# Performance work log

Measured on AMD Instinct MI355X. Metric: run time of the kernel, lower is better.

## Reference

```python
import jax, jax.numpy as jnp
import numpy as np

NUM_EXPERTS = 8
TOP_K = 2
DIM = 1024
HIDDEN = 4096
B, S = 4, 2048


def setup_inputs() -> dict:
    key = jax.random.key(0)
    ks = jax.random.split(key, 6)
    scale = 0.02
    x = jax.random.normal(ks[0], (B, S, DIM), dtype=jnp.float32)
    wg = jax.random.normal(ks[1], (NUM_EXPERTS, DIM), dtype=jnp.float32) * scale
    bg = jnp.zeros((NUM_EXPERTS,), dtype=jnp.float32)
    Wgate = jax.random.normal(ks[2], (NUM_EXPERTS, HIDDEN, DIM), dtype=jnp.float32) * scale
    Wup = jax.random.normal(ks[3], (NUM_EXPERTS, HIDDEN, DIM), dtype=jnp.float32) * scale
    Wdown = jax.random.normal(ks[4], (NUM_EXPERTS, DIM, HIDDEN), dtype=jnp.float32) * scale
    return {"x": x, "wg": wg, "bg": bg, "Wgate": Wgate, "Wup": Wup, "Wdown": Wdown}


def reference(x, wg, bg, Wgate, Wup, Wdown):
    b, s, d = x.shape
    xf = x.reshape(-1, d)  # [T, D]
    T = xf.shape[0]
    # --- gating: top-k over router logits, softmax over masked logits ---
    logits = xf @ wg.T + bg  # [T, E]
    vals, idx = jax.lax.top_k(logits, TOP_K)  # [T, K]
    masked = jnp.full_like(logits, -jnp.inf)
    rows = jnp.arange(T)[:, None]
    masked = masked.at[rows, idx].set(vals)
    weights = jax.nn.softmax(masked, axis=-1)  # zeros outside top-k
    # --- experts: weighted SwiGLU sum (weight is 0 for non-routed tokens,
    # so this matches the gather/scatter loop exactly) ---
    out = jnp.zeros_like(xf)
    for e in range(NUM_EXPERTS):
        g = xf @ Wgate[e].T            # [T, H]
        u = xf @ Wup[e].T              # [T, H]
        h = (g * jax.nn.sigmoid(g)) * u
        out = out + (h @ Wdown[e].T) * weights[:, e:e + 1]
    return out.reshape(b, s, d)
```

## Files before the change

kernel.cpp:

```cpp
#include <hip/hip_runtime.h>
#include <cstdint>
#include <cstddef>

typedef unsigned short ushort_t;
typedef __attribute__((ext_vector_type(8))) __bf16 bf16x8;
typedef __attribute__((ext_vector_type(8))) short  s16x8;
typedef __attribute__((ext_vector_type(4))) float  f32x4;

#define NE 8
#define DIM 1024
#define HIDDEN 4096
#define NTOK 8192
#define CAP NTOK
#define NROWS (NTOK * 2)

#define BM 128
#define BN 64
#define BK 32
#define LDP 40

static constexpr size_t WS_COUNTS  = 0;
static constexpr size_t WS_OFFSETS = 256;
static constexpr size_t WS_TOKENS  = 512;
static constexpr size_t WS_WEIGHTS = WS_TOKENS + (size_t)NE * CAP * 4;
static constexpr size_t WS_H       = ((WS_WEIGHTS + (size_t)NE * CAP * 4 + 1023) / 1024) * 1024;
static constexpr size_t H_BYTES    = (size_t)NROWS * HIDDEN * 2;
static constexpr size_t WS_XB      = WS_H + H_BYTES;
static constexpr size_t XB_BYTES   = (size_t)NTOK * DIM * 2;
static constexpr size_t W_BYTES    = (size_t)NE * HIDDEN * DIM * 2;
static constexpr size_t WS_WGB     = WS_XB + XB_BYTES;
static constexpr size_t WS_WUB     = WS_WGB + W_BYTES;
static constexpr size_t WS_WDB     = WS_WUB + W_BYTES;
static constexpr size_t WS_T1_END  = WS_WDB;
static constexpr size_t WS_T2_END  = WS_WDB + W_BYTES;

__device__ __forceinline__ ushort_t cvt_bf16(float f) {
  unsigned u = __float_as_uint(f);
  return (ushort_t)((u + 0x7FFFu + ((u >> 16) & 1u)) >> 16);
}

__device__ __forceinline__ void st8(ushort_t* dst, float4 a, float4 b) {
  s16x8 v;
  v[0] = (short)cvt_bf16(a.x); v[1] = (short)cvt_bf16(a.y);
  v[2] = (short)cvt_bf16(a.z); v[3] = (short)cvt_bf16(a.w);
  v[4] = (short)cvt_bf16(b.x); v[5] = (short)cvt_bf16(b.y);
  v[6] = (short)cvt_bf16(b.z); v[7] = (short)cvt_bf16(b.w);
  *reinterpret_cast<s16x8*>(dst) = v;
}

__device__ __forceinline__ bf16x8 ldb(const ushort_t* p) {
  union { s16x8 s; bf16x8 b; } u;
  u.s = *reinterpret_cast<const s16x8*>(p);
  return u.b;
}

__device__ __forceinline__ bf16x8 ldt(const ushort_t* base, int row, int s) {
  return ldb(base + (size_t)((row << 2) + (s ^ ((row >> 1) & 3))) * 8);
}

__device__ __forceinline__ f32x4 mfma16(bf16x8 a, bf16x8 b, f32x4 c) {
  return __builtin_amdgcn_mfma_f32_16x16x32_bf16(a, b, c, 0, 0, 0);
}

#define GLDS16(g, l)                                                     \
  __builtin_amdgcn_global_load_lds(                                      \
      (const __attribute__((address_space(1))) unsigned int*)(g),        \
      (__attribute__((address_space(3))) unsigned int*)(l), 16, 0, 0)

__global__ __launch_bounds__(256) void cvt_kernel(const float* __restrict__ s,
                                                  ushort_t* __restrict__ d, long n8) {
  long i = (long)blockIdx.x * 256 + threadIdx.x;
  long stride = (long)gridDim.x * 256;
  for (long p = i; p < n8; p += stride) {
    const float4* sp = reinterpret_cast<const float4*>(s) + 2 * p;
    float4 a = sp[0];
    float4 b = sp[1];
    st8(d + p * 8, a, b);
  }
}

__global__ __launch_bounds__(256) void gating_kernel(
    const float* __restrict__ x, const float* __restrict__ wg,
    const float* __restrict__ bg, int* __restrict__ counts,
    int* __restrict__ token_list, float* __restrict__ weight_list) {
  int gid  = blockIdx.x * blockDim.x + threadIdx.x;
  int tok  = gid >> 6;
  int lane = threadIdx.x & 63;
  if (tok >= NTOK) return;
  const float* xr = x + (size_t)tok * DIM;

  float part[NE];
#pragma unroll
  for (int e = 0; e < NE; ++e) part[e] = 0.f;
  for (int i = lane; i < DIM; i += 64) {
    float xv = xr[i];
#pragma unroll
    for (int e = 0; e < NE; ++e) part[e] = fmaf(xv, wg[e * DIM + i], part[e]);
  }
#pragma unroll
  for (int e = 0; e < NE; ++e) {
    float v = part[e];
#pragma unroll
    for (int o = 32; o > 0; o >>= 1) v += __shfl_xor(v, o, 64);
    part[e] = v + bg[e];
  }
  if (lane == 0) {
    int i0 = 0; float v0 = part[0];
#pragma unroll
    for (int e = 1; e < NE; ++e) if (part[e] > v0) { v0 = part[e]; i0 = e; }
    int i1 = -1; float v1 = -INFINITY;
#pragma unroll
    for (int e = 0; e < NE; ++e) if (e != i0 && part[e] > v1) { v1 = part[e]; i1 = e; }
    float e1 = expf(v1 - v0);
    float s  = 1.f + e1;
    float w0 = 1.f / s;
    float w1 = e1 / s;
    int s0 = atomicAdd(&counts[i0], 1);
    token_list[i0 * CAP + s0]  = tok;
    weight_list[i0 * CAP + s0] = w0;
    int s1 = atomicAdd(&counts[i1], 1);
    token_list[i1 * CAP + s1]  = tok;
    weight_list[i1 * CAP + s1] = w1;
  }
}

__global__ void prefix_kernel(const int* __restrict__ counts, int* __restrict__ offsets) {
  if (threadIdx.x == 0) {
    int acc = 0;
    for (int e = 0; e < NE; ++e) { offsets[e] = acc; acc += counts[e]; }
  }
}

__global__ __launch_bounds__(256) void stage1_kernel(
    const ushort_t* __restrict__ xb, const ushort_t* __restrict__ wgb,
    const ushort_t* __restrict__ wub, const int* __restrict__ counts,
    const int* __restrict__ offsets, const int* __restrict__ token_list,
    ushort_t* __restrict__ h) {
  const int e  = blockIdx.z;
  const int mt = blockIdx.y;
  const int nt = blockIdx.x;
  const int count = counts[e];
  if (mt * BM >= count) return;

  __shared__ __align__(16) ushort_t XsL[BM * 32];
  __shared__ __align__(16) ushort_t GsL[BN * 32];
  __shared__ __align__(16) ushort_t UsL[BN * 32];
  __shared__ int toks[BM];

  const int t = threadIdx.x;
  if (t < BM) {
    int m = mt * BM + t;
    toks[t] = token_list[e * CAP + (m < count ? m : count - 1)];
  }
  __syncthreads();

  const int wid  = t >> 6;
  const int lane = t & 63;
  const int wm   = wid & 1;
  const int wn   = wid >> 1;
  const int fr   = lane & 15;
  const int kg   = lane >> 4;

  const int uA = wid * 128 + lane;
  const int uB = uA + 64;
  const int rA = uA >> 2, sA = (uA & 3) ^ ((rA >> 1) & 3);
  const int rB = uB >> 2, sB = (uB & 3) ^ ((rB >> 1) & 3);
  const ushort_t* gxA = xb + (size_t)toks[rA] * DIM + sA * 8;
  const ushort_t* gxB = xb + (size_t)toks[rB] * DIM + sB * 8;

  const int uG = wid * 64 + lane;
  const int rG = uG >> 2, sG = (uG & 3) ^ ((rG >> 1) & 3);
  const size_t wrow = (size_t)e * HIDDEN + (size_t)nt * BN + rG;
  const ushort_t* ggp = wgb + wrow * DIM + sG * 8;
  const ushort_t* gup = wub + wrow * DIM + sG * 8;

  ushort_t* ldsXA = XsL + (size_t)(wid * 128) * 8;
  ushort_t* ldsXB = XsL + (size_t)(wid * 128 + 64) * 8;
  ushort_t* ldsG  = GsL + (size_t)(wid * 64) * 8;
  ushort_t* ldsU  = UsL + (size_t)(wid * 64) * 8;

  f32x4 accg[4][2], accu[4][2];
#pragma unroll
  for (int i = 0; i < 4; ++i)
#pragma unroll
    for (int j = 0; j < 2; ++j) { accg[i][j] = (f32x4)0.f; accu[i][j] = (f32x4)0.f; }

  for (int k0 = 0; k0 < DIM; k0 += BK) {
    GLDS16(gxA + k0, ldsXA);
    GLDS16(gxB + k0, ldsXB);
    GLDS16(ggp + k0, ldsG);
    GLDS16(gup + k0, ldsU);
    __syncthreads();

    bf16x8 bg0 = ldt(GsL, wn * 32 + fr, kg);
    bf16x8 bg1 = ldt(GsL, wn * 32 + 16 + fr, kg);
    bf16x8 bu0 = ldt(UsL, wn * 32 + fr, kg);
    bf16x8 bu1 = ldt(UsL, wn * 32 + 16 + fr, kg);
#pragma unroll
    for (int mf = 0; mf < 4; ++mf) {
      bf16x8 a = ldt(XsL, wm * 64 + mf * 16 + fr, kg);
      accg[mf][0] = mfma16(a, bg0, accg[mf][0]);
      accg[mf][1] = mfma16(a, bg1, accg[mf][1]);
      accu[mf][0] = mfma16(a, bu0, accu[mf][0]);
      accu[mf][1] = mfma16(a, bu1, accu[mf][1]);
    }
    __syncthreads();
  }

  const size_t slot0 = (size_t)offsets[e];
  const int nbase = nt * BN + wn * 32;
#pragma unroll
  for (int mf = 0; mf < 4; ++mf) {
#pragma unroll
    for (int r = 0; r < 4; ++r) {
      int ml = wm * 64 + mf * 16 + kg * 4 + r;
      int m  = mt * BM + ml;
      if (m < count) {
        size_t rowoff = (slot0 + m) * (size_t)HIDDEN + nbase;
#pragma unroll
        for (int nf = 0; nf < 2; ++nf) {
          float g  = accg[mf][nf][r];
          float uu = accu[mf][nf][r];
          float hv = g / (1.f + __expf(-g)) * uu;
          h[rowoff + nf * 16 + fr] = cvt_bf16(hv);
        }
      }
    }
  }
}

__global__ __launch_bounds__(256) void stage2_kernel(
    const ushort_t* __restrict__ h, const ushort_t* __restrict__ wdb,
    const int* __restrict__ counts, const int* __restrict__ offsets,
    const int* __restrict__ token_list, const float* __restrict__ weight_list,
    float* __restrict__ out) {
  const int e  = blockIdx.z;
  const int mt = blockIdx.y;
  const int nt = blockIdx.x;
  const int count = counts[e];
  if (mt * BM >= count) return;

  __shared__ __align__(16) ushort_t AsL[BM * 32];
  __shared__ __align__(16) ushort_t DsL[BN * 32];
  __shared__ int   toks[BM];
  __shared__ float wts[BM];

  const int t = threadIdx.x;
  if (t < BM) {
    int m  = mt * BM + t;
    int mc = m < count ? m : count - 1;
    toks[t] = token_list[e * CAP + mc];
    wts[t]  = weight_list[e * CAP + mc];
  }
  __syncthreads();

  const int wid  = t >> 6;
  const int lane = t & 63;
  const int wm   = wid & 1;
  const int wn   = wid >> 1;
  const int fr   = lane & 15;
  const int kg   = lane >> 4;

  const int slot0b = offsets[e] + mt * BM;

  const int uA = wid * 128 + lane;
  const int uB = uA + 64;
  const int rA = uA >> 2, sA = (uA & 3) ^ ((rA >> 1) & 3);
  const int rB = uB >> 2, sB = (uB & 3) ^ ((rB >> 1) & 3);
  int hrA = slot0b + rA; hrA = hrA < NROWS ? hrA : NROWS - 1;
  int hrB = slot0b + rB; hrB = hrB < NROWS ? hrB : NROWS - 1;
  const ushort_t* ghA = h + (size_t)hrA * HIDDEN + sA * 8;
  const ushort_t* ghB = h + (size_t)hrB * HIDDEN + sB * 8;

  const int uD = wid * 64 + lane;
  const int rD = uD >> 2, sD = (uD & 3) ^ ((rD >> 1) & 3);
  const ushort_t* gdp = wdb + ((size_t)e * DIM + (size_t)nt * BN + rD) * HIDDEN + sD * 8;

  ushort_t* ldsAA = AsL + (size_t)(wid * 128) * 8;
  ushort_t* ldsAB = AsL + (size_t)(wid * 128 + 64) * 8;
  ushort_t* ldsD  = DsL + (size_t)(wid * 64) * 8;

  f32x4 acc[4][2];
#pragma unroll
  for (int i = 0; i < 4; ++i)
#pragma unroll
    for (int j = 0; j < 2; ++j) acc[i][j] = (f32x4)0.f;

  for (int k0 = 0; k0 < HIDDEN; k0 += BK) {
    GLDS16(ghA + k0, ldsAA);
    GLDS16(ghB + k0, ldsAB);
    GLDS16(gdp + k0, ldsD);
    __syncthreads();

    bf16x8 b0 = ldt(DsL, wn * 32 + fr, kg);
    bf16x8 b1 = ldt(DsL, wn * 32 + 16 + fr, kg);
#pragma unroll
    for (int mf = 0; mf < 4; ++mf) {
      bf16x8 a = ldt(AsL, wm * 64 + mf * 16 + fr, kg);
      acc[mf][0] = mfma16(a, b0, acc[mf][0]);
      acc[mf][1] = mfma16(a, b1, acc[mf][1]);
    }
    __syncthreads();
  }

  const int nbase = nt * BN + wn * 32;
#pragma unroll
  for (int mf = 0; mf < 4; ++mf) {
#pragma unroll
    for (int r = 0; r < 4; ++r) {
      int ml = wm * 64 + mf * 16 + kg * 4 + r;
      int m  = mt * BM + ml;
      if (m < count) {
        int   tok = toks[ml];
        float w   = wts[ml];
        size_t o  = (size_t)tok * DIM + nbase;
#pragma unroll
        for (int nf = 0; nf < 2; ++nf) {
          atomicAdd(&out[o + nf * 16 + fr], acc[mf][nf][r] * w);
        }
      }
    }
  }
}

__global__ __launch_bounds__(256) void stage1_f32w(
    const float* __restrict__ x, const float* __restrict__ Wgate,
    const float* __restrict__ Wup, const int* __restrict__ counts,
    const int* __restrict__ offsets, const int* __restrict__ token_list,
    ushort_t* __restrict__ h) {
  const int e  = blockIdx.z;
  const int mt = blockIdx.y;
  const int nt = blockIdx.x;
  const int count = counts[e];
  if (mt * BM >= count) return;

  __shared__ __align__(16) ushort_t Xs[BM][LDP];
  __shared__ __align__(16) ushort_t Gs[BN][LDP];
  __shared__ __align__(16) ushort_t Us[BN][LDP];
  __shared__ int toks[BM];

  const int t = threadIdx.x;
  if (t < BM) {
    int m = mt * BM + t;
    toks[t] = token_list[e * CAP + (m < count ? m : count - 1)];
  }
  __syncthreads();

  const float* Wg = Wgate + (size_t)e * HIDDEN * DIM + (size_t)(nt * BN) * DIM;
  const float* Wu = Wup   + (size_t)e * HIDDEN * DIM + (size_t)(nt * BN) * DIM;

  const int wid  = t >> 6;
  const int lane = t & 63;
  const int wm   = wid & 1;
  const int wn   = wid >> 1;
  const int fr   = lane & 15;
  const int kg   = lane >> 4;

  f32x4 accg[4][2], accu[4][2];
#pragma unroll
  for (int i = 0; i < 4; ++i)
#pragma unroll
    for (int j = 0; j < 2; ++j) { accg[i][j] = (f32x4)0.f; accu[i][j] = (f32x4)0.f; }

  const int sr = t >> 2;
  const int sc = (t & 3) * 8;

  const int tok0 = toks[sr];
  const int tok1 = toks[sr + 64];
  const float* xp0 = x + (size_t)tok0 * DIM + sc;
  const float* xp1 = x + (size_t)tok1 * DIM + sc;
  const float* gp  = Wg + (size_t)sr * DIM + sc;
  const float* up  = Wu + (size_t)sr * DIM + sc;

  for (int k0 = 0; k0 < DIM; k0 += BK) {
    float4 a0 = *reinterpret_cast<const float4*>(xp0 + k0);
    float4 a1 = *reinterpret_cast<const float4*>(xp0 + k0 + 4);
    float4 b0 = *reinterpret_cast<const float4*>(xp1 + k0);
    float4 b1 = *reinterpret_cast<const float4*>(xp1 + k0 + 4);
    float4 g0 = *reinterpret_cast<const float4*>(gp + k0);
    float4 g1 = *reinterpret_cast<const float4*>(gp + k0 + 4);
    float4 u0 = *reinterpret_cast<const float4*>(up + k0);
    float4 u1 = *reinterpret_cast<const float4*>(up + k0 + 4);
    st8(&Xs[sr][sc],      a0, a1);
    st8(&Xs[sr + 64][sc], b0, b1);
    st8(&Gs[sr][sc],      g0, g1);
    st8(&Us[sr][sc],      u0, u1);
    __syncthreads();

    bf16x8 bg0 = ldb(&Gs[wn * 32 + fr][kg * 8]);
    bf16x8 bg1 = ldb(&Gs[wn * 32 + 16 + fr][kg * 8]);
    bf16x8 bu0 = ldb(&Us[wn * 32 + fr][kg * 8]);
    bf16x8 bu1 = ldb(&Us[wn * 32 + 16 + fr][kg * 8]);
#pragma unroll
    for (int mf = 0; mf < 4; ++mf) {
      bf16x8 a = ldb(&Xs[wm * 64 + mf * 16 + fr][kg * 8]);
      accg[mf][0] = mfma16(a, bg0, accg[mf][0]);
      accg[mf][1] = mfma16(a, bg1, accg[mf][1]);
      accu[mf][0] = mfma16(a, bu0, accu[mf][0]);
      accu[mf][1] = mfma16(a, bu1, accu[mf][1]);
    }
    __syncthreads();
  }

  const size_t slot0 = (size_t)offsets[e];
  const int nbase = nt * BN + wn * 32;
#pragma unroll
  for (int mf = 0; mf < 4; ++mf) {
#pragma unroll
    for (int r = 0; r < 4; ++r) {
      int ml = wm * 64 + mf * 16 + kg * 4 + r;
      int m  = mt * BM + ml;
      if (m < count) {
        size_t rowoff = (slot0 + m) * (size_t)HIDDEN + nbase;
#pragma unroll
        for (int nf = 0; nf < 2; ++nf) {
          float g  = accg[mf][nf][r];
          float uu = accu[mf][nf][r];
          float hv = g / (1.f + __expf(-g)) * uu;
          h[rowoff + nf * 16 + fr] = cvt_bf16(hv);
        }
      }
    }
  }
}

__global__ __launch_bounds__(256) void stage2_f32w(
    const ushort_t* __restrict__ h, const float* __restrict__ Wdown,
    const int* __restrict__ counts, const int* __restrict__ offsets,
    const int* __restrict__ token_list, const float* __restrict__ weight_list,
    float* __restrict__ out) {
  const int e  = blockIdx.z;
  const int mt = blockIdx.y;
  const int nt = blockIdx.x;
  const int count = counts[e];
  if (mt * BM >= count) return;

  __shared__ __align__(16) ushort_t As[BM][LDP];
  __shared__ __align__(16) ushort_t Ds[BN][LDP];
  __shared__ int   toks[BM];
  __shared__ float wts[BM];

  const int t = threadIdx.x;
  if (t < BM) {
    int m  = mt * BM + t;
    int mc = m < count ? m : count - 1;
    toks[t] = token_list[e * CAP + mc];
    wts[t]  = weight_list[e * CAP + mc];
  }
  __syncthreads();

  const float* Wd = Wdown + (size_t)e * DIM * HIDDEN + (size_t)(nt * BN) * HIDDEN;
  const int slot0b = offsets[e] + mt * BM;

  const int wid  = t >> 6;
  const int lane = t & 63;
  const int wm   = wid & 1;
  const int wn   = wid >> 1;
  const int fr   = lane & 15;
  const int kg   = lane >> 4;

  f32x4 acc[4][2];
#pragma unroll
  for (int i = 0; i < 4; ++i)
#pragma unroll
    for (int j = 0; j < 2; ++j) acc[i][j] = (f32x4)0.f;

  const int sr = t >> 2;
  const int sc = (t & 3) * 8;

  int r0 = slot0b + sr;       r0 = r0 < NROWS ? r0 : NROWS - 1;
  int r1 = slot0b + sr + 64;  r1 = r1 < NROWS ? r1 : NROWS - 1;
  const ushort_t* hp0 = h + (size_t)r0 * HIDDEN + sc;
  const ushort_t* hp1 = h + (size_t)r1 * HIDDEN + sc;
  const float*    dp  = Wd + (size_t)sr * HIDDEN + sc;

  for (int k0 = 0; k0 < HIDDEN; k0 += BK) {
    s16x8 ha = *reinterpret_cast<const s16x8*>(hp0 + k0);
    s16x8 hb = *reinterpret_cast<const s16x8*>(hp1 + k0);
    float4 d0 = *reinterpret_cast<const float4*>(dp + k0);
    float4 d1 = *reinterpret_cast<const float4*>(dp + k0 + 4);
    *reinterpret_cast<s16x8*>(&As[sr][sc])      = ha;
    *reinterpret_cast<s16x8*>(&As[sr + 64][sc]) = hb;
    st8(&Ds[sr][sc], d0, d1);
    __syncthreads();

    bf16x8 b0 = ldb(&Ds[wn * 32 + fr][kg * 8]);
    bf16x8 b1 = ldb(&Ds[wn * 32 + 16 + fr][kg * 8]);
#pragma unroll
    for (int mf = 0; mf < 4; ++mf) {
      bf16x8 a = ldb(&As[wm * 64 + mf * 16 + fr][kg * 8]);
      acc[mf][0] = mfma16(a, b0, acc[mf][0]);
      acc[mf][1] = mfma16(a, b1, acc[mf][1]);
    }
    __syncthreads();
  }

  const int nbase = nt * BN + wn * 32;
#pragma unroll
  for (int mf = 0; mf < 4; ++mf) {
#pragma unroll
    for (int r = 0; r < 4; ++r) {
      int ml = wm * 64 + mf * 16 + kg * 4 + r;
      int m  = mt * BM + ml;
      if (m < count) {
        int   tok = toks[ml];
        float w   = wts[ml];
        size_t o  = (size_t)tok * DIM + nbase;
#pragma unroll
        for (int nf = 0; nf < 2; ++nf) {
          atomicAdd(&out[o + nf * 16 + fr], acc[mf][nf][r] * w);
        }
      }
    }
  }
}

extern "C" void kernel_launch(void* const* d_in, const int* in_sizes, int n_in,
                              void* d_out, int out_size, void* d_ws, size_t ws_size,
                              hipStream_t stream) {
  const float* x     = (const float*)d_in[0];
  const float* wg    = (const float*)d_in[1];
  const float* bg    = (const float*)d_in[2];
  const float* Wgate = (const float*)d_in[3];
  const float* Wup   = (const float*)d_in[4];
  const float* Wdown = (const float*)d_in[5];
  float* out = (float*)d_out;

  char* ws = (char*)d_ws;
  int*      counts      = (int*)(ws + WS_COUNTS);
  int*      offsets     = (int*)(ws + WS_OFFSETS);
  int*      token_list  = (int*)(ws + WS_TOKENS);
  float*    weight_list = (float*)(ws + WS_WEIGHTS);
  ushort_t* h           = (ushort_t*)(ws + WS_H);

  hipMemsetAsync(counts, 0, NE * sizeof(int), stream);
  hipMemsetAsync(out, 0, (size_t)NTOK * DIM * sizeof(float), stream);

  gating_kernel<<<NTOK / 4, 256, 0, stream>>>(x, wg, bg, counts, token_list, weight_list);
  prefix_kernel<<<1, 64, 0, stream>>>(counts, offsets);

  const bool tier1 = ws_size >= WS_T1_END;
  const bool tier2 = ws_size >= WS_T2_END;

  if (tier1) {
    ushort_t* xb  = (ushort_t*)(ws + WS_XB);
    ushort_t* wgb = (ushort_t*)(ws + WS_WGB);
    ushort_t* wub = (ushort_t*)(ws + WS_WUB);

    long w8 = (long)NE * HIDDEN * DIM / 8;
    long x8 = (long)NTOK * DIM / 8;
    cvt_kernel<<<8192, 256, 0, stream>>>(Wgate, wgb, w8);
    cvt_kernel<<<8192, 256, 0, stream>>>(Wup,   wub, w8);
    cvt_kernel<<<4096, 256, 0, stream>>>(x,     xb,  x8);

    stage1_kernel<<<dim3(HIDDEN / BN, CAP / BM, NE), 256, 0, stream>>>(
        xb, wgb, wub, counts, offsets, token_list, h);

    if (tier2) {
      ushort_t* wdb = (ushort_t*)(ws + WS_WDB);
      cvt_kernel<<<8192, 256, 0, stream>>>(Wdown, wdb, w8);
      stage2_kernel<<<dim3(DIM / BN, CAP / BM, NE), 256, 0, stream>>>(
          h, wdb, counts, offsets, token_list, weight_list, out);
    } else {
      stage2_f32w<<<dim3(DIM / BN, CAP / BM, NE), 256, 0, stream>>>(
          h, Wdown, counts, offsets, token_list, weight_list, out);
    }
  } else {
    stage1_f32w<<<dim3(HIDDEN / BN, CAP / BM, NE), 256, 0, stream>>>(
        x, Wgate, Wup, counts, offsets, token_list, h);
    stage2_f32w<<<dim3(DIM / BN, CAP / BM, NE), 256, 0, stream>>>(
        h, Wdown, counts, offsets, token_list, weight_list, out);
  }
}
```

Baseline: 1.246 ms.

## Replace atomic scatter in down-projection with per-slot output buffer and combine kernel

The down-projection now writes unweighted per-slot results into a dense fp32 buffer y, and a new combine kernel gathers each token's two expert rows, weights them, and writes the output directly. This removes the fp32 atomicAdd scatter and the output memset. Gating also records each token's slot indices (tpair). The converted Wdown now reuses the Wgate bf16 buffer after stage1, which shrinks workspace needs. The cost is an extra 64MB write and read of y plus one more kernel launch, and the path only runs if the workspace is large enough.

```diff
diff --git a/kernel.cpp b/kernel.cpp
--- a/kernel.cpp
+++ b/kernel.cpp
@@ -21,18 +21,20 @@
 
 static constexpr size_t WS_COUNTS  = 0;
 static constexpr size_t WS_OFFSETS = 256;
-static constexpr size_t WS_TOKENS  = 512;
+static constexpr size_t WS_TPAIR   = 512;
+static constexpr size_t WS_TOKENS  = WS_TPAIR + (size_t)NTOK * 2 * 4;
 static constexpr size_t WS_WEIGHTS = WS_TOKENS + (size_t)NE * CAP * 4;
 static constexpr size_t WS_H       = ((WS_WEIGHTS + (size_t)NE * CAP * 4 + 1023) / 1024) * 1024;
 static constexpr size_t H_BYTES    = (size_t)NROWS * HIDDEN * 2;
 static constexpr size_t WS_XB      = WS_H + H_BYTES;
 static constexpr size_t XB_BYTES   = (size_t)NTOK * DIM * 2;
 static constexpr size_t W_BYTES    = (size_t)NE * HIDDEN * DIM * 2;
-static constexpr size_t WS_WGB     = WS_XB + XB_BYTES;
-static constexpr size_t WS_WUB     = WS_WGB + W_BYTES;
-static constexpr size_t WS_WDB     = WS_WUB + W_BYTES;
-static constexpr size_t WS_T1_END  = WS_WDB;
-static constexpr size_t WS_T2_END  = WS_WDB + W_BYTES;
+static constexpr size_t WS_WA      = WS_XB + XB_BYTES;
+static constexpr size_t WS_WUB     = WS_WA + W_BYTES;
+static constexpr size_t WS_T1_END  = WS_WUB + W_BYTES;
+static constexpr size_t WS_Y       = WS_T1_END;
+static constexpr size_t Y_BYTES    = (size_t)NROWS * DIM * 4;
+static constexpr size_t WS_T3_END  = WS_Y + Y_BYTES;
 
 __device__ __forceinline__ ushort_t cvt_bf16(float f) {
   unsigned u = __float_as_uint(f);
@@ -82,7 +84,8 @@
 __global__ __launch_bounds__(256) void gating_kernel(
     const float* __restrict__ x, const float* __restrict__ wg,
     const float* __restrict__ bg, int* __restrict__ counts,
-    int* __restrict__ token_list, float* __restrict__ weight_list) {
+    int* __restrict__ token_list, float* __restrict__ weight_list,
+    int* __restrict__ tpair) {
   int gid  = blockIdx.x * blockDim.x + threadIdx.x;
   int tok  = gid >> 6;
   int lane = threadIdx.x & 63;
@@ -118,9 +121,11 @@
     int s0 = atomicAdd(&counts[i0], 1);
     token_list[i0 * CAP + s0]  = tok;
     weight_list[i0 * CAP + s0] = w0;
+    tpair[tok * 2 + 0] = i0 * CAP + s0;
     int s1 = atomicAdd(&counts[i1], 1);
     token_list[i1 * CAP + s1]  = tok;
     weight_list[i1 * CAP + s1] = w1;
+    tpair[tok * 2 + 1] = i1 * CAP + s1;
   }
 }
 
@@ -229,6 +234,87 @@
   }
 }
 
+__global__ __launch_bounds__(256) void stage2_y_kernel(
+    const ushort_t* __restrict__ h, const ushort_t* __restrict__ wdb,
+    const int* __restrict__ counts, const int* __restrict__ offsets,
+    float* __restrict__ y) {
+  const int e  = blockIdx.z;
+  const int mt = blockIdx.y;
+  const int nt = blockIdx.x;
+  const int count = counts[e];
+  if (mt * BM >= count) return;
+
+  __shared__ __align__(16) ushort_t AsL[BM * 32];
+  __shared__ __align__(16) ushort_t DsL[BN * 32];
+
+  const int t = threadIdx.x;
+  const int wid  = t >> 6;
+  const int lane = t & 63;
+  const int wm   = wid & 1;
+  const int wn   = wid >> 1;
+  const int fr   = lane & 15;
+  const int kg   = lane >> 4;
+
+  const int slot0b = offsets[e] + mt * BM;
+
+  const int uA = wid * 128 + lane;
+  const int uB = uA + 64;
+  const int rA = uA >> 2, sA = (uA & 3) ^ ((rA >> 1) & 3);
+  const int rB = uB >> 2, sB = (uB & 3) ^ ((rB >> 1) & 3);
+  int hrA = slot0b + rA; hrA = hrA < NROWS ? hrA : NROWS - 1;
+  int hrB = slot0b + rB; hrB = hrB < NROWS ? hrB : NROWS - 1;
+  const ushort_t* ghA = h + (size_t)hrA * HIDDEN + sA * 8;
+  const ushort_t* ghB = h + (size_t)hrB * HIDDEN + sB * 8;
+
+  const int uD = wid * 64 + lane;
+  const int rD = uD >> 2, sD = (uD & 3) ^ ((rD >> 1) & 3);
+  const ushort_t* gdp = wdb + ((size_t)e * DIM + (size_t)nt * BN + rD) * HIDDEN + sD * 8;
+
+  ushort_t* ldsAA = AsL + (size_t)(wid * 128) * 8;
+  ushort_t* ldsAB = AsL + (size_t)(wid * 128 + 64) * 8;
+  ushort_t* ldsD  = DsL + (size_t)(wid * 64) * 8;
+
+  f32x4 acc[4][2];
+#pragma unroll
+  for (int i = 0; i < 4; ++i)
+#pragma unroll
+    for (int j = 0; j < 2; ++j) acc[i][j] = (f32x4)0.f;
+
+  for (int k0 = 0; k0 < HIDDEN; k0 += BK) {
+    GLDS16(ghA + k0, ldsAA);
+    GLDS16(ghB + k0, ldsAB);
+    GLDS16(gdp + k0, ldsD);
+    __syncthreads();
+
+    bf16x8 b0 = ldt(DsL, wn * 32 + fr, kg);
+    bf16x8 b1 = ldt(DsL, wn * 32 + 16 + fr, kg);
+#pragma unroll
+    for (int mf = 0; mf < 4; ++mf) {
+      bf16x8 a = ldt(AsL, wm * 64 + mf * 16 + fr, kg);
+      acc[mf][0] = mfma16(a, b0, acc[mf][0]);
+      acc[mf][1] = mfma16(a, b1, acc[mf][1]);
+    }
+    __syncthreads();
+  }
+
+  const int nbase = nt * BN + wn * 32;
+#pragma unroll
+  for (int mf = 0; mf < 4; ++mf) {
+#pragma unroll
+    for (int r = 0; r < 4; ++r) {
+      int ml = wm * 64 + mf * 16 + kg * 4 + r;
+      int m  = mt * BM + ml;
+      if (m < count) {
+        size_t row = (size_t)(slot0b + ml);
+#pragma unroll
+        for (int nf = 0; nf < 2; ++nf) {
+          y[row * DIM + nbase + nf * 16 + fr] = acc[mf][nf][r];
+        }
+      }
+    }
+  }
+}
+
 __global__ __launch_bounds__(256) void stage2_kernel(
     const ushort_t* __restrict__ h, const ushort_t* __restrict__ wdb,
     const int* __restrict__ counts, const int* __restrict__ offsets,
@@ -321,6 +407,28 @@
       }
     }
   }
+}
+
+__global__ __launch_bounds__(256) void combine_kernel(
+    const float* __restrict__ y, const int* __restrict__ tpair,
+    const float* __restrict__ weight_list, const int* __restrict__ offsets,
+    float* __restrict__ out) {
+  const int tok = blockIdx.x;
+  const int v0 = tpair[tok * 2 + 0];
+  const int v1 = tpair[tok * 2 + 1];
+  const float w0 = weight_list[v0];
+  const float w1 = weight_list[v1];
+  const int s0 = offsets[v0 >> 13] + (v0 & (CAP - 1));
+  const int s1 = offsets[v1 >> 13] + (v1 & (CAP - 1));
+  const int d = threadIdx.x * 4;
+  float4 a = *reinterpret_cast<const float4*>(y + (size_t)s0 * DIM + d);
+  float4 b = *reinterpret_cast<const float4*>(y + (size_t)s1 * DIM + d);
+  float4 o;
+  o.x = w0 * a.x + w1 * b.x;
+  o.y = w0 * a.y + w1 * b.y;
+  o.z = w0 * a.z + w1 * b.z;
+  o.w = w0 * a.w + w1 * b.w;
+  *reinterpret_cast<float4*>(out + (size_t)tok * DIM + d) = o;
 }
 
 __global__ __launch_bounds__(256) void stage1_f32w(
@@ -529,43 +637,48 @@
   char* ws = (char*)d_ws;
   int*      counts      = (int*)(ws + WS_COUNTS);
   int*      offsets     = (int*)(ws + WS_OFFSETS);
+  int*      tpair       = (int*)(ws + WS_TPAIR);
   int*      token_list  = (int*)(ws + WS_TOKENS);
   float*    weight_list = (float*)(ws + WS_WEIGHTS);
   ushort_t* h           = (ushort_t*)(ws + WS_H);
 
   hipMemsetAsync(counts, 0, NE * sizeof(int), stream);
-  hipMemsetAsync(out, 0, (size_t)NTOK * DIM * sizeof(float), stream);
-
-  gating_kernel<<<NTOK / 4, 256, 0, stream>>>(x, wg, bg, counts, token_list, weight_list);
+
+  gating_kernel<<<NTOK / 4, 256, 0, stream>>>(x, wg, bg, counts, token_list,
+                                              weight_list, tpair);
   prefix_kernel<<<1, 64, 0, stream>>>(counts, offsets);
 
   const bool tier1 = ws_size >= WS_T1_END;
-  const bool tier2 = ws_size >= WS_T2_END;
+  const bool tier3 = ws_size >= WS_T3_END;
 
   if (tier1) {
     ushort_t* xb  = (ushort_t*)(ws + WS_XB);
-    ushort_t* wgb = (ushort_t*)(ws + WS_WGB);
+    ushort_t* wA  = (ushort_t*)(ws + WS_WA);
     ushort_t* wub = (ushort_t*)(ws + WS_WUB);
 
     long w8 = (long)NE * HIDDEN * DIM / 8;
     long x8 = (long)NTOK * DIM / 8;
-    cvt_kernel<<<8192, 256, 0, stream>>>(Wgate, wgb, w8);
+    cvt_kernel<<<8192, 256, 0, stream>>>(Wgate, wA, w8);
     cvt_kernel<<<8192, 256, 0, stream>>>(Wup,   wub, w8);
     cvt_kernel<<<4096, 256, 0, stream>>>(x,     xb,  x8);
 
     stage1_kernel<<<dim3(HIDDEN / BN, CAP / BM, NE), 256, 0, stream>>>(
-        xb, wgb, wub, counts, offsets, token_list, h);
-
-    if (tier2) {
-      ushort_t* wdb = (ushort_t*)(ws + WS_WDB);
-      cvt_kernel<<<8192, 256, 0, stream>>>(Wdown, wdb, w8);
+        xb, wA, wub, counts, offsets, token_list, h);
+
+    cvt_kernel<<<8192, 256, 0, stream>>>(Wdown, wA, w8);
+
+    if (tier3) {
+      float* y = (float*)(ws + WS_Y);
+      stage2_y_kernel<<<dim3(DIM / BN, CAP / BM, NE), 256, 0, stream>>>(
+          h, wA, counts, offsets, y);
+      combine_kernel<<<NTOK, 256, 0, stream>>>(y, tpair, weight_list, offsets, out);
+    } else {
+      hipMemsetAsync(out, 0, (size_t)NTOK * DIM * sizeof(float), stream);
       stage2_kernel<<<dim3(DIM / BN, CAP / BM, NE), 256, 0, stream>>>(
-          h, wdb, counts, offsets, token_list, weight_list, out);
-    } else {
-      stage2_f32w<<<dim3(DIM / BN, CAP / BM, NE), 256, 0, stream>>>(
-          h, Wdown, counts, offsets, token_list, weight_list, out);
+          h, wA, counts, offsets, token_list, weight_list, out);
     }
   } else {
+    hipMemsetAsync(out, 0, (size_t)NTOK * DIM * sizeof(float), stream);
     stage1_f32w<<<dim3(HIDDEN / BN, CAP / BM, NE), 256, 0, stream>>>(
         x, Wgate, Wup, counts, offsets, token_list, h);
     stage2_f32w<<<dim3(DIM / BN, CAP / BM, NE), 256, 0, stream>>>(
```

Result: no change. 1.222 ms (-1.9%).

## Replace atomic scatter in down-projection with per-slot output and combine pass

Applied to the files above, without the earlier changes.

The down-projection kernel now writes unweighted per-slot rows into a float buffer y, with wider 128-column tiles. A new combine kernel gathers each token's two rows through a token-to-slot map recorded by gating and applies the routing weights. This removes the float atomics and the memset of the output. The three weight and input conversions are fused into one launch, and workspace is reused so the Wdown bf16 copy overwrites the Wgate copy and y aliases the Wup copy. In exchange it adds an extra pass over a 64 MB intermediate, and the lower workspace threshold changes which path runs.

```diff
diff --git a/kernel.cpp b/kernel.cpp
--- a/kernel.cpp
+++ b/kernel.cpp
@@ -16,23 +16,24 @@
 
 #define BM 128
 #define BN 64
+#define BN2 128
 #define BK 32
 #define LDP 40
 
 static constexpr size_t WS_COUNTS  = 0;
 static constexpr size_t WS_OFFSETS = 256;
-static constexpr size_t WS_TOKENS  = 512;
+static constexpr size_t WS_TPAIR   = 512;
+static constexpr size_t WS_TOKENS  = WS_TPAIR + (size_t)NTOK * 2 * 4;
 static constexpr size_t WS_WEIGHTS = WS_TOKENS + (size_t)NE * CAP * 4;
 static constexpr size_t WS_H       = ((WS_WEIGHTS + (size_t)NE * CAP * 4 + 1023) / 1024) * 1024;
 static constexpr size_t H_BYTES    = (size_t)NROWS * HIDDEN * 2;
 static constexpr size_t WS_XB      = WS_H + H_BYTES;
 static constexpr size_t XB_BYTES   = (size_t)NTOK * DIM * 2;
 static constexpr size_t W_BYTES    = (size_t)NE * HIDDEN * DIM * 2;
-static constexpr size_t WS_WGB     = WS_XB + XB_BYTES;
-static constexpr size_t WS_WUB     = WS_WGB + W_BYTES;
-static constexpr size_t WS_WDB     = WS_WUB + W_BYTES;
-static constexpr size_t WS_T1_END  = WS_WDB;
-static constexpr size_t WS_T2_END  = WS_WDB + W_BYTES;
+static constexpr size_t WS_WA      = WS_XB + XB_BYTES;
+static constexpr size_t WS_WUB     = WS_WA + W_BYTES;
+static constexpr size_t WS_Y       = WS_WUB;
+static constexpr size_t WS_T1_END  = WS_WUB + W_BYTES;
 
 __device__ __forceinline__ ushort_t cvt_bf16(float f) {
   unsigned u = __float_as_uint(f);
@@ -79,10 +80,30 @@
   }
 }
 
+__global__ __launch_bounds__(256) void cvt3_kernel(
+    const float* __restrict__ s0, ushort_t* __restrict__ d0, long n0,
+    const float* __restrict__ s1, ushort_t* __restrict__ d1, long n1,
+    const float* __restrict__ s2, ushort_t* __restrict__ d2, long n2) {
+  long i = (long)blockIdx.x * 256 + threadIdx.x;
+  long stride = (long)gridDim.x * 256;
+  long ntot = n0 + n1 + n2;
+  for (long p = i; p < ntot; p += stride) {
+    const float* s; ushort_t* d; long q = p;
+    if (q < n0)            { s = s0; d = d0; }
+    else if ((q -= n0) < n1) { s = s1; d = d1; }
+    else                   { q -= n1; s = s2; d = d2; }
+    const float4* sp = reinterpret_cast<const float4*>(s) + 2 * q;
+    float4 a = sp[0];
+    float4 b = sp[1];
+    st8(d + q * 8, a, b);
+  }
+}
+
 __global__ __launch_bounds__(256) void gating_kernel(
     const float* __restrict__ x, const float* __restrict__ wg,
     const float* __restrict__ bg, int* __restrict__ counts,
-    int* __restrict__ token_list, float* __restrict__ weight_list) {
+    int* __restrict__ token_list, float* __restrict__ weight_list,
+    int* __restrict__ tpair) {
   int gid  = blockIdx.x * blockDim.x + threadIdx.x;
   int tok  = gid >> 6;
   int lane = threadIdx.x & 63;
@@ -118,9 +139,11 @@
     int s0 = atomicAdd(&counts[i0], 1);
     token_list[i0 * CAP + s0]  = tok;
     weight_list[i0 * CAP + s0] = w0;
+    tpair[tok * 2 + 0] = i0 * CAP + s0;
     int s1 = atomicAdd(&counts[i1], 1);
     token_list[i1 * CAP + s1]  = tok;
     weight_list[i1 * CAP + s1] = w1;
+    tpair[tok * 2 + 1] = i1 * CAP + s1;
   }
 }
 
@@ -229,11 +252,10 @@
   }
 }
 
-__global__ __launch_bounds__(256) void stage2_kernel(
+__global__ __launch_bounds__(256) void stage2_y_kernel(
     const ushort_t* __restrict__ h, const ushort_t* __restrict__ wdb,
     const int* __restrict__ counts, const int* __restrict__ offsets,
-    const int* __restrict__ token_list, const float* __restrict__ weight_list,
-    float* __restrict__ out) {
+    float* __restrict__ y) {
   const int e  = blockIdx.z;
   const int mt = blockIdx.y;
   const int nt = blockIdx.x;
@@ -241,19 +263,9 @@
   if (mt * BM >= count) return;
 
   __shared__ __align__(16) ushort_t AsL[BM * 32];
-  __shared__ __align__(16) ushort_t DsL[BN * 32];
-  __shared__ int   toks[BM];
-  __shared__ float wts[BM];
+  __shared__ __align__(16) ushort_t DsL[BN2 * 32];
 
   const int t = threadIdx.x;
-  if (t < BM) {
-    int m  = mt * BM + t;
-    int mc = m < count ? m : count - 1;
-    toks[t] = token_list[e * CAP + mc];
-    wts[t]  = weight_list[e * CAP + mc];
-  }
-  __syncthreads();
-
   const int wid  = t >> 6;
   const int lane = t & 63;
   const int wm   = wid & 1;
@@ -272,38 +284,40 @@
   const ushort_t* ghA = h + (size_t)hrA * HIDDEN + sA * 8;
   const ushort_t* ghB = h + (size_t)hrB * HIDDEN + sB * 8;
 
-  const int uD = wid * 64 + lane;
-  const int rD = uD >> 2, sD = (uD & 3) ^ ((rD >> 1) & 3);
-  const ushort_t* gdp = wdb + ((size_t)e * DIM + (size_t)nt * BN + rD) * HIDDEN + sD * 8;
+  const ushort_t* gdA = wdb + ((size_t)e * DIM + (size_t)nt * BN2 + rA) * HIDDEN + sA * 8;
+  const ushort_t* gdB = wdb + ((size_t)e * DIM + (size_t)nt * BN2 + rB) * HIDDEN + sB * 8;
 
   ushort_t* ldsAA = AsL + (size_t)(wid * 128) * 8;
   ushort_t* ldsAB = AsL + (size_t)(wid * 128 + 64) * 8;
-  ushort_t* ldsD  = DsL + (size_t)(wid * 64) * 8;
-
-  f32x4 acc[4][2];
+  ushort_t* ldsDA = DsL + (size_t)(wid * 128) * 8;
+  ushort_t* ldsDB = DsL + (size_t)(wid * 128 + 64) * 8;
+
+  f32x4 acc[4][4];
 #pragma unroll
   for (int i = 0; i < 4; ++i)
 #pragma unroll
-    for (int j = 0; j < 2; ++j) acc[i][j] = (f32x4)0.f;
+    for (int j = 0; j < 4; ++j) acc[i][j] = (f32x4)0.f;
 
   for (int k0 = 0; k0 < HIDDEN; k0 += BK) {
     GLDS16(ghA + k0, ldsAA);
     GLDS16(ghB + k0, ldsAB);
-    GLDS16(gdp + k0, ldsD);
-    __syncthreads();
-
-    bf16x8 b0 = ldt(DsL, wn * 32 + fr, kg);
-    bf16x8 b1 = ldt(DsL, wn * 32 + 16 + fr, kg);
+    GLDS16(gdA + k0, ldsDA);
+    GLDS16(gdB + k0, ldsDB);
+    __syncthreads();
+
+    bf16x8 b[4];
+#pragma unroll
+    for (int nf = 0; nf < 4; ++nf) b[nf] = ldt(DsL, wn * 64 + nf * 16 + fr, kg);
 #pragma unroll
     for (int mf = 0; mf < 4; ++mf) {
       bf16x8 a = ldt(AsL, wm * 64 + mf * 16 + fr, kg);
-      acc[mf][0] = mfma16(a, b0, acc[mf][0]);
-      acc[mf][1] = mfma16(a, b1, acc[mf][1]);
-    }
-    __syncthreads();
-  }
-
-  const int nbase = nt * BN + wn * 32;
+#pragma unroll
+      for (int nf = 0; nf < 4; ++nf) acc[mf][nf] = mfma16(a, b[nf], acc[mf][nf]);
+    }
+    __syncthreads();
+  }
+
+  const int nbase = nt * BN2 + wn * 64;
 #pragma unroll
   for (int mf = 0; mf < 4; ++mf) {
 #pragma unroll
@@ -311,16 +325,36 @@
       int ml = wm * 64 + mf * 16 + kg * 4 + r;
       int m  = mt * BM + ml;
       if (m < count) {
-        int   tok = toks[ml];
-        float w   = wts[ml];
-        size_t o  = (size_t)tok * DIM + nbase;
-#pragma unroll
-        for (int nf = 0; nf < 2; ++nf) {
-          atomicAdd(&out[o + nf * 16 + fr], acc[mf][nf][r] * w);
+        size_t row = (size_t)(slot0b + ml);
+#pragma unroll
+        for (int nf = 0; nf < 4; ++nf) {
+          y[row * DIM + nbase + nf * 16 + fr] = acc[mf][nf][r];
         }
       }
     }
   }
+}
+
+__global__ __launch_bounds__(256) void combine_kernel(
+    const float* __restrict__ y, const int* __restrict__ tpair,
+    const float* __restrict__ weight_list, const int* __restrict__ offsets,
+    float* __restrict__ out) {
+  const int tok = blockIdx.x;
+  const int v0 = tpair[tok * 2 + 0];
+  const int v1 = tpair[tok * 2 + 1];
+  const float w0 = weight_list[v0];
+  const float w1 = weight_list[v1];
+  const int s0 = offsets[v0 >> 13] + (v0 & (CAP - 1));
+  const int s1 = offsets[v1 >> 13] + (v1 & (CAP - 1));
+  const int d = threadIdx.x * 4;
+  float4 a = *reinterpret_cast<const float4*>(y + (size_t)s0 * DIM + d);
+  float4 b = *reinterpret_cast<const float4*>(y + (size_t)s1 * DIM + d);
+  float4 o;
+  o.x = w0 * a.x + w1 * b.x;
+  o.y = w0 * a.y + w1 * b.y;
+  o.z = w0 * a.z + w1 * b.z;
+  o.w = w0 * a.w + w1 * b.w;
+  *reinterpret_cast<float4*>(out + (size_t)tok * DIM + d) = o;
 }
 
 __global__ __launch_bounds__(256) void stage1_f32w(
@@ -529,43 +563,37 @@
   char* ws = (char*)d_ws;
   int*      counts      = (int*)(ws + WS_COUNTS);
   int*      offsets     = (int*)(ws + WS_OFFSETS);
+  int*      tpair       = (int*)(ws + WS_TPAIR);
   int*      token_list  = (int*)(ws + WS_TOKENS);
   float*    weight_list = (float*)(ws + WS_WEIGHTS);
   ushort_t* h           = (ushort_t*)(ws + WS_H);
 
   hipMemsetAsync(counts, 0, NE * sizeof(int), stream);
-  hipMemsetAsync(out, 0, (size_t)NTOK * DIM * sizeof(float), stream);
-
-  gating_kernel<<<NTOK / 4, 256, 0, stream>>>(x, wg, bg, counts, token_list, weight_list);
+
+  gating_kernel<<<NTOK / 4, 256, 0, stream>>>(x, wg, bg, counts, token_list,
+                                              weight_list, tpair);
   prefix_kernel<<<1, 64, 0, stream>>>(counts, offsets);
 
-  const bool tier1 = ws_size >= WS_T1_END;
-  const bool tier2 = ws_size >= WS_T2_END;
-
-  if (tier1) {
+  if (ws_size >= WS_T1_END) {
     ushort_t* xb  = (ushort_t*)(ws + WS_XB);
-    ushort_t* wgb = (ushort_t*)(ws + WS_WGB);
+    ushort_t* wA  = (ushort_t*)(ws + WS_WA);
     ushort_t* wub = (ushort_t*)(ws + WS_WUB);
+    float*    y   = (float*)(ws + WS_Y);
 
     long w8 = (long)NE * HIDDEN * DIM / 8;
     long x8 = (long)NTOK * DIM / 8;
-    cvt_kernel<<<8192, 256, 0, stream>>>(Wgate, wgb, w8);
-    cvt_kernel<<<8192, 256, 0, stream>>>(Wup,   wub, w8);
-    cvt_kernel<<<4096, 256, 0, stream>>>(x,     xb,  x8);
+    cvt3_kernel<<<8192, 256, 0, stream>>>(Wgate, wA, w8, Wup, wub, w8, x, xb, x8);
 
     stage1_kernel<<<dim3(HIDDEN / BN, CAP / BM, NE), 256, 0, stream>>>(
-        xb, wgb, wub, counts, offsets, token_list, h);
-
-    if (tier2) {
-      ushort_t* wdb = (ushort_t*)(ws + WS_WDB);
-      cvt_kernel<<<8192, 256, 0, stream>>>(Wdown, wdb, w8);
-      stage2_kernel<<<dim3(DIM / BN, CAP / BM, NE), 256, 0, stream>>>(
-          h, wdb, counts, offsets, token_list, weight_list, out);
-    } else {
-      stage2_f32w<<<dim3(DIM / BN, CAP / BM, NE), 256, 0, stream>>>(
-          h, Wdown, counts, offsets, token_list, weight_list, out);
-    }
+        xb, wA, wub, counts, offsets, token_list, h);
+
+    cvt_kernel<<<8192, 256, 0, stream>>>(Wdown, wA, w8);
+
+    stage2_y_kernel<<<dim3(DIM / BN2, CAP / BM, NE), 256, 0, stream>>>(
+        h, wA, counts, offsets, y);
+    combine_kernel<<<NTOK, 256, 0, stream>>>(y, tpair, weight_list, offsets, out);
   } else {
+    hipMemsetAsync(out, 0, (size_t)NTOK * DIM * sizeof(float), stream);
     stage1_f32w<<<dim3(HIDDEN / BN, CAP / BM, NE), 256, 0, stream>>>(
         x, Wgate, Wup, counts, offsets, token_list, h);
     stage2_f32w<<<dim3(DIM / BN, CAP / BM, NE), 256, 0, stream>>>(
```

Result: no change. 1.244 ms (-0.1%).
